# Optimization experiments

Hardware: AMD Instinct MI355X
Metric: run time of the kernel (lower is better)

Reference implementation:

```python
import jax, jax.numpy as jnp
import numpy as np

FT_IN = 40960   # HalfKP-style feature space
FFT_IN = 640    # factorized piece-square features
FT_OUT = 256


def setup_inputs() -> dict:
    key = jax.random.key(0)
    ks = jax.random.split(key, 10)
    B, A = 16384, 30  # batch, active features per board
    inp = {
        "stm_idx": jax.random.randint(ks[0], (B, A), 0, FT_IN, dtype=jnp.int32),
        "nstm_idx": jax.random.randint(ks[1], (B, A), 0, FT_IN, dtype=jnp.int32),
        "f_stm_idx": jax.random.randint(ks[2], (B, A), 0, FFT_IN, dtype=jnp.int32),
        "f_nstm_idx": jax.random.randint(ks[3], (B, A), 0, FFT_IN, dtype=jnp.int32),
        # learned parameters (glorot-ish scale)
        "ft_w": jax.random.normal(ks[4], (FT_IN, FT_OUT), jnp.float32) * 0.01,
        "ft_b": jax.random.normal(ks[5], (FT_OUT,), jnp.float32) * 0.01,
        "fft_w": jax.random.normal(ks[6], (FFT_IN, FT_OUT), jnp.float32) * 0.05,
        "fft_b": jax.random.normal(ks[7], (FT_OUT,), jnp.float32) * 0.01,
        "out_w": jax.random.normal(ks[8], (2 * FT_OUT, 1), jnp.float32) * 0.05,
        "out_b": jax.random.normal(ks[9], (1,), jnp.float32) * 0.01,
    }
    return inp


def _accumulate(w, b, idx):
    # sparse one-hot board @ kernel + bias == gather rows and sum over active features
    return jnp.take(w, idx, axis=0).sum(axis=1) + b  # [B, FT_OUT]


def reference(stm_idx, nstm_idx, f_stm_idx, f_nstm_idx,
              ft_w, ft_b, fft_w, fft_b, out_w, out_b):
    stm = _accumulate(ft_w, ft_b, stm_idx)        # [B, 256]
    nstm = _accumulate(ft_w, ft_b, nstm_idx)      # [B, 256]
    f_stm = _accumulate(fft_w, fft_b, f_stm_idx)  # [B, 256]
    f_nstm = _accumulate(fft_w, fft_b, f_nstm_idx)
    merge = jnp.concatenate((stm, nstm), axis=1) + jnp.concatenate((f_stm, f_nstm), axis=1)
    h = jnp.clip(merge, 0.0, 1.0)                 # ReLU(max_value=1.0)
    return jax.nn.sigmoid(h @ out_w + out_b)      # [B, 1]
```

## Files before the change

### kernel.cpp

```cpp
#include <hip/hip_runtime.h>
#include <math.h>

#define FT_IN  40960
#define FFT_IN 640
#define FT_OUT 256
#define NA     30
#define NSLICE 4
#define BPB    128

typedef float f32x2 __attribute__((ext_vector_type(2)));

__device__ __forceinline__ unsigned enc4(float a, float b, float c, float d) {
    unsigned r = 0;
    r = __builtin_amdgcn_cvt_pk_fp8_f32(a, b, r, false);
    r = __builtin_amdgcn_cvt_pk_fp8_f32(c, d, r, true);
    return r;
}

__device__ __forceinline__ void conv8_block(const float* __restrict__ src,
                                            uint4* __restrict__ dst,
                                            int nrows, int bid, int tid)
{
    int t = bid * 256 + tid;
    int total = nrows * 16;
    if (t >= total) return;
    int r = t >> 4, g = t & 15;
    int s = g >> 2, d = g & 3;
    const float4* sp = (const float4*)(src + (size_t)r * FT_OUT + g * 16);
    float4 v0 = sp[0], v1 = sp[1], v2 = sp[2], v3 = sp[3];
    uint4 u;
    u.x = enc4(v0.x, v0.y, v0.z, v0.w);
    u.y = enc4(v1.x, v1.y, v1.z, v1.w);
    u.z = enc4(v2.x, v2.y, v2.z, v2.w);
    u.w = enc4(v3.x, v3.y, v3.z, v3.w);
    dst[((size_t)s * nrows + r) * 4 + d] = u;
}

__global__ __launch_bounds__(256) void prep(
    const float* __restrict__ ft_w, const float* __restrict__ fft_w,
    const int* __restrict__ stm, const int* __restrict__ nstm,
    const int* __restrict__ fstm, const int* __restrict__ fnstm,
    uint4* __restrict__ ft_o, uint4* __restrict__ fft_o,
    uint2* __restrict__ pidx, int n_boards, int nb_ft, int nb_fft)
{
    int bid = blockIdx.x;
    if (bid < nb_ft) {
        conv8_block(ft_w, ft_o, FT_IN, bid, threadIdx.x);
    } else if (bid < nb_ft + nb_fft) {
        conv8_block(fft_w, fft_o, FFT_IN, bid - nb_ft, threadIdx.x);
    } else {
        int t = (bid - nb_ft - nb_fft) * 256 + (int)threadIdx.x;
        int total = n_boards * NA;
        if (t < total) {
            uint2 v;
            v.x = (unsigned)stm[t]  | ((unsigned)nstm[t]  << 16);
            v.y = (unsigned)fstm[t] | ((unsigned)fnstm[t] << 16);
            pidx[t] = v;
        }
    }
}

__global__ __launch_bounds__(1024, 8) void nnue_gather(
    const uint2* __restrict__ pidx,
    const char* __restrict__ ft, const char* __restrict__ fft,
    const float* __restrict__ ft_b, const float* __restrict__ fft_b,
    const float* __restrict__ out_w, float* __restrict__ partial, int n_boards)
{
    extern __shared__ char smem[];
    uint2* lidx = (uint2*)smem;
    uint2* lf8  = (uint2*)(smem + NA * BPB * 8);
    const int slice = blockIdx.x & (NSLICE - 1);
    const int group = blockIdx.x >> 2;
    const int tid = (int)threadIdx.x;

    {
        const uint2* psrc = pidx + (size_t)group * BPB * NA;
        int lim = (n_boards - group * BPB) * NA;
        if (lim > NA * BPB) lim = NA * BPB;
        for (int i = tid; i < lim; i += 1024)
            lidx[i] = psrc[i];
    }
    {
        const uint2* fsrc = (const uint2*)(fft + (size_t)slice * FFT_IN * 64);
        for (int i = tid; i < FFT_IN * 8; i += 1024) {
            int r = i >> 3, c = i & 7;
            lf8[(r << 3) + ((c + r) & 7)] = fsrc[i];
        }
    }
    __syncthreads();

    const int sub = tid >> 3, ql = tid & 7;
    int board = group * BPB + sub;
    const bool active = board < n_boards;
    const char* ftS = ft + (size_t)slice * FT_IN * 64 + ql * 8;
    const int col = slice * 64 + ql * 8;

    f32x2 a0[4] = {f32x2{0.f,0.f}, f32x2{0.f,0.f}, f32x2{0.f,0.f}, f32x2{0.f,0.f}};
    f32x2 a1[4] = {f32x2{0.f,0.f}, f32x2{0.f,0.f}, f32x2{0.f,0.f}, f32x2{0.f,0.f}};

    const uint2* myidx = lidx + sub * NA;

    #pragma unroll
    for (int a = 0; a < NA; ++a) {
        uint2 iv = myidx[a];
        uint2 u0 = *(const uint2*)(ftS + ((iv.x & 0xFFFFu) << 6));
        uint2 u1 = *(const uint2*)(ftS + ((iv.x >> 16) << 6));
        unsigned rz = iv.y & 0xFFFFu, rw = iv.y >> 16;
        uint2 g0 = lf8[(rz << 3) + (((unsigned)ql + rz) & 7)];
        uint2 g1 = lf8[(rw << 3) + (((unsigned)ql + rw) & 7)];
        a0[0] += __builtin_amdgcn_cvt_pk_f32_fp8(u0.x, false);
        a0[1] += __builtin_amdgcn_cvt_pk_f32_fp8(u0.x, true);
        a0[2] += __builtin_amdgcn_cvt_pk_f32_fp8(u0.y, false);
        a0[3] += __builtin_amdgcn_cvt_pk_f32_fp8(u0.y, true);
        a1[0] += __builtin_amdgcn_cvt_pk_f32_fp8(u1.x, false);
        a1[1] += __builtin_amdgcn_cvt_pk_f32_fp8(u1.x, true);
        a1[2] += __builtin_amdgcn_cvt_pk_f32_fp8(u1.y, false);
        a1[3] += __builtin_amdgcn_cvt_pk_f32_fp8(u1.y, true);
        a0[0] += __builtin_amdgcn_cvt_pk_f32_fp8(g0.x, false);
        a0[1] += __builtin_amdgcn_cvt_pk_f32_fp8(g0.x, true);
        a0[2] += __builtin_amdgcn_cvt_pk_f32_fp8(g0.y, false);
        a0[3] += __builtin_amdgcn_cvt_pk_f32_fp8(g0.y, true);
        a1[0] += __builtin_amdgcn_cvt_pk_f32_fp8(g1.x, false);
        a1[1] += __builtin_amdgcn_cvt_pk_f32_fp8(g1.x, true);
        a1[2] += __builtin_amdgcn_cvt_pk_f32_fp8(g1.y, false);
        a1[3] += __builtin_amdgcn_cvt_pk_f32_fp8(g1.y, true);
    }

    const float4* bfp = (const float4*)(ft_b  + col);
    const float4* bgp = (const float4*)(fft_b + col);
    float4 bf0 = bfp[0], bf1 = bfp[1], bg0 = bgp[0], bg1 = bgp[1];
    float bias[8] = {bf0.x+bg0.x, bf0.y+bg0.y, bf0.z+bg0.z, bf0.w+bg0.w,
                     bf1.x+bg1.x, bf1.y+bg1.y, bf1.z+bg1.z, bf1.w+bg1.w};
    const float4* w0p = (const float4*)(out_w + col);
    const float4* w1p = (const float4*)(out_w + FT_OUT + col);
    float4 w00 = w0p[0], w01 = w0p[1], w10 = w1p[0], w11 = w1p[1];
    float w0[8] = {w00.x, w00.y, w00.z, w00.w, w01.x, w01.y, w01.z, w01.w};
    float w1[8] = {w10.x, w10.y, w10.z, w10.w, w11.x, w11.y, w11.z, w11.w};
    float h0[8], h1[8];
    #pragma unroll
    for (int i = 0; i < 4; ++i) {
        h0[2*i] = a0[i].x; h0[2*i+1] = a0[i].y;
        h1[2*i] = a1[i].x; h1[2*i+1] = a1[i].y;
    }
    float p = 0.f;
    #pragma unroll
    for (int i = 0; i < 8; ++i) {
        p += fminf(fmaxf(h0[i] + bias[i], 0.f), 1.f) * w0[i];
        p += fminf(fmaxf(h1[i] + bias[i], 0.f), 1.f) * w1[i];
    }
    p += __shfl_xor(p, 1, 64);
    p += __shfl_xor(p, 2, 64);
    p += __shfl_xor(p, 4, 64);
    if (active && ql == 0)
        partial[(size_t)slice * n_boards + board] = p;
}

__global__ __launch_bounds__(256) void nnue_final(
    const float* __restrict__ partial, const float* __restrict__ out_b,
    float* __restrict__ out, int n)
{
    int b = blockIdx.x * blockDim.x + threadIdx.x;
    if (b >= n) return;
    float zv = out_b[0];
    #pragma unroll
    for (int s = 0; s < NSLICE; ++s) zv += partial[(size_t)s * n + b];
    out[b] = 1.0f / (1.0f + expf(-zv));
}

__global__ __launch_bounds__(256) void nnue_fwd_direct(
    const int* __restrict__ stm_idx, const int* __restrict__ nstm_idx,
    const int* __restrict__ f_stm_idx, const int* __restrict__ f_nstm_idx,
    const float* __restrict__ ft_w, const float* __restrict__ ft_b,
    const float* __restrict__ fft_w, const float* __restrict__ fft_b,
    const float* __restrict__ out_w, const float* __restrict__ out_b,
    float* __restrict__ out, int n_boards)
{
    const int board = (int)((blockIdx.x * blockDim.x + threadIdx.x) >> 6);
    const int lane  = (int)(threadIdx.x & 63);
    if (board >= n_boards) return;
    const int col = lane << 2;
    const float4 ftb  = *(const float4*)(ft_b  + col);
    const float4 fftb = *(const float4*)(fft_b + col);
    float a0x = ftb.x + fftb.x, a0y = ftb.y + fftb.y,
          a0z = ftb.z + fftb.z, a0w = ftb.w + fftb.w;
    float a1x = a0x, a1y = a0y, a1z = a0z, a1w = a0w;
    const int* si  = stm_idx    + (size_t)board * NA;
    const int* ni  = nstm_idx   + (size_t)board * NA;
    const int* fsi = f_stm_idx  + (size_t)board * NA;
    const int* fni = f_nstm_idx + (size_t)board * NA;
    #pragma unroll 5
    for (int a = 0; a < NA; ++a) {
        const float4 r0 = *(const float4*)(ft_w  + (size_t)si[a]  * FT_OUT + col);
        const float4 r1 = *(const float4*)(ft_w  + (size_t)ni[a]  * FT_OUT + col);
        const float4 r2 = *(const float4*)(fft_w + (size_t)fsi[a] * FT_OUT + col);
        const float4 r3 = *(const float4*)(fft_w + (size_t)fni[a] * FT_OUT + col);
        a0x += r0.x + r2.x; a0y += r0.y + r2.y; a0z += r0.z + r2.z; a0w += r0.w + r2.w;
        a1x += r1.x + r3.x; a1y += r1.y + r3.y; a1z += r1.z + r3.z; a1w += r1.w + r3.w;
    }
    a0x = fminf(fmaxf(a0x, 0.f), 1.f); a0y = fminf(fmaxf(a0y, 0.f), 1.f);
    a0z = fminf(fmaxf(a0z, 0.f), 1.f); a0w = fminf(fmaxf(a0w, 0.f), 1.f);
    a1x = fminf(fmaxf(a1x, 0.f), 1.f); a1y = fminf(fmaxf(a1y, 0.f), 1.f);
    a1z = fminf(fmaxf(a1z, 0.f), 1.f); a1w = fminf(fmaxf(a1w, 0.f), 1.f);
    const float4 w0 = *(const float4*)(out_w + col);
    const float4 w1 = *(const float4*)(out_w + FT_OUT + col);
    float p = a0x * w0.x + a0y * w0.y + a0z * w0.z + a0w * w0.w
            + a1x * w1.x + a1y * w1.y + a1z * w1.z + a1w * w1.w;
    #pragma unroll
    for (int off = 32; off > 0; off >>= 1) p += __shfl_down(p, off, 64);
    if (lane == 0) out[board] = 1.0f / (1.0f + expf(-(p + out_b[0])));
}

extern "C" void kernel_launch(void* const* d_in, const int* in_sizes, int n_in,
                              void* d_out, int out_size, void* d_ws, size_t ws_size,
                              hipStream_t stream) {
    const int*   stm_idx    = (const int*)d_in[0];
    const int*   nstm_idx   = (const int*)d_in[1];
    const int*   f_stm_idx  = (const int*)d_in[2];
    const int*   f_nstm_idx = (const int*)d_in[3];
    const float* ft_w  = (const float*)d_in[4];
    const float* ft_b  = (const float*)d_in[5];
    const float* fft_w = (const float*)d_in[6];
    const float* fft_b = (const float*)d_in[7];
    const float* out_w = (const float*)d_in[8];
    const float* out_b = (const float*)d_in[9];
    float* out = (float*)d_out;

    const int n_boards = in_sizes[0] / NA;

    const size_t ft_bytes   = (size_t)FT_IN  * FT_OUT;
    const size_t fft_bytes  = (size_t)FFT_IN * FT_OUT;
    const size_t pidx_bytes = (size_t)n_boards * NA * sizeof(uint2);
    const size_t part_bytes = (size_t)n_boards * NSLICE * sizeof(float);
    const size_t need = ft_bytes + fft_bytes + pidx_bytes + part_bytes;

    const size_t lds_bytes = (size_t)NA * BPB * 8 + (size_t)FFT_IN * 64;

    bool ok = (ws_size >= need);
    if (ok) {
        ok = (hipFuncSetAttribute((const void*)nnue_gather,
                                  hipFuncAttributeMaxDynamicSharedMemorySize,
                                  (int)lds_bytes) == hipSuccess);
    }
    if (!ok) {
        const int grid = (n_boards + 3) / 4;
        nnue_fwd_direct<<<grid, 256, 0, stream>>>(stm_idx, nstm_idx, f_stm_idx, f_nstm_idx,
                                                  ft_w, ft_b, fft_w, fft_b, out_w, out_b,
                                                  out, n_boards);
        return;
    }

    char* wsp = (char*)d_ws;
    uint4* ws_ft   = (uint4*)wsp;               wsp += ft_bytes;
    uint4* ws_fft  = (uint4*)wsp;               wsp += fft_bytes;
    uint2* ws_pidx = (uint2*)wsp;               wsp += pidx_bytes;
    float* ws_part = (float*)wsp;

    {
        const int nb_ft   = FT_IN  * 16 / 256;
        const int nb_fft  = FFT_IN * 16 / 256;
        const int nb_pack = (n_boards * NA + 255) / 256;
        prep<<<nb_ft + nb_fft + nb_pack, 256, 0, stream>>>(
            ft_w, fft_w, stm_idx, nstm_idx, f_stm_idx, f_nstm_idx,
            ws_ft, ws_fft, ws_pidx, n_boards, nb_ft, nb_fft);
    }
    {
        int groups = (n_boards + BPB - 1) / BPB;
        nnue_gather<<<groups * NSLICE, 1024, lds_bytes, stream>>>(
            (const uint2*)ws_pidx, (const char*)ws_ft, (const char*)ws_fft,
            ft_b, fft_b, out_w, ws_part, n_boards);
    }
    {
        nnue_final<<<(n_boards + 255) / 256, 256, 0, stream>>>(ws_part, out_b, out, n_boards);
    }
}
```

Before: 132.9 us.

## Drop LDS staging of factorized weights and split lanes by side with 16-byte loads

The gather kernel no longer copies the factorized fp8 weight slice into LDS. Instead, each lane loads 16-byte rows of both tables directly from global memory, and lanes are split between the stm and nstm sides, with each lane covering 16 columns of one side. Blocks shrink from 1024 threads and 128 boards to 256 threads and 32 boards, with static LDS used only for indices. This removes the per-block LDS fill of 40KB and the dynamic-LDS setup, and should raise occupancy. The trade-off is that factorized-weight reads now go through L2/L1 instead of LDS.

New measurement: 136.6 us. 2.8% more time.

```diff
diff --git a/kernel.cpp b/kernel.cpp
--- a/kernel.cpp
+++ b/kernel.cpp
@@ -6,7 +6,7 @@
 #define FT_OUT 256
 #define NA     30
 #define NSLICE 4
-#define BPB    128
+#define BPB    32
 
 typedef float f32x2 __attribute__((ext_vector_type(2)));
 
@@ -60,15 +60,13 @@
     }
 }
 
-__global__ __launch_bounds__(1024, 8) void nnue_gather(
+__global__ __launch_bounds__(256, 5) void nnue_gather(
     const uint2* __restrict__ pidx,
     const char* __restrict__ ft, const char* __restrict__ fft,
     const float* __restrict__ ft_b, const float* __restrict__ fft_b,
     const float* __restrict__ out_w, float* __restrict__ partial, int n_boards)
 {
-    extern __shared__ char smem[];
-    uint2* lidx = (uint2*)smem;
-    uint2* lf8  = (uint2*)(smem + NA * BPB * 8);
+    __shared__ uint2 lidx[BPB * NA];
     const int slice = blockIdx.x & (NSLICE - 1);
     const int group = blockIdx.x >> 2;
     const int tid = (int)threadIdx.x;
@@ -77,76 +75,68 @@
         const uint2* psrc = pidx + (size_t)group * BPB * NA;
         int lim = (n_boards - group * BPB) * NA;
         if (lim > NA * BPB) lim = NA * BPB;
-        for (int i = tid; i < lim; i += 1024)
-            lidx[i] = psrc[i];
-    }
-    {
-        const uint2* fsrc = (const uint2*)(fft + (size_t)slice * FFT_IN * 64);
-        for (int i = tid; i < FFT_IN * 8; i += 1024) {
-            int r = i >> 3, c = i & 7;
-            lf8[(r << 3) + ((c + r) & 7)] = fsrc[i];
-        }
+        for (int i = tid; i < NA * BPB; i += 256)
+            lidx[i] = (i < lim) ? psrc[i] : uint2{0u, 0u};
     }
     __syncthreads();
 
-    const int sub = tid >> 3, ql = tid & 7;
-    int board = group * BPB + sub;
+    const int sub  = tid >> 3;
+    const int ql   = tid & 7;
+    const int side = ql >> 2;
+    const int c    = ql & 3;
+    const unsigned shf = (unsigned)side << 4;
+    const int board = group * BPB + sub;
     const bool active = board < n_boards;
-    const char* ftS = ft + (size_t)slice * FT_IN * 64 + ql * 8;
-    const int col = slice * 64 + ql * 8;
-
-    f32x2 a0[4] = {f32x2{0.f,0.f}, f32x2{0.f,0.f}, f32x2{0.f,0.f}, f32x2{0.f,0.f}};
-    f32x2 a1[4] = {f32x2{0.f,0.f}, f32x2{0.f,0.f}, f32x2{0.f,0.f}, f32x2{0.f,0.f}};
+
+    const char* ftS  = ft  + (size_t)slice * FT_IN  * 64 + c * 16;
+    const char* fftS = fft + (size_t)slice * FFT_IN * 64 + c * 16;
+    const int col = slice * 64 + c * 16;
+
+    f32x2 acc[8];
+    #pragma unroll
+    for (int i = 0; i < 8; ++i) acc[i] = f32x2{0.f, 0.f};
 
     const uint2* myidx = lidx + sub * NA;
 
     #pragma unroll
     for (int a = 0; a < NA; ++a) {
         uint2 iv = myidx[a];
-        uint2 u0 = *(const uint2*)(ftS + ((iv.x & 0xFFFFu) << 6));
-        uint2 u1 = *(const uint2*)(ftS + ((iv.x >> 16) << 6));
-        unsigned rz = iv.y & 0xFFFFu, rw = iv.y >> 16;
-        uint2 g0 = lf8[(rz << 3) + (((unsigned)ql + rz) & 7)];
-        uint2 g1 = lf8[(rw << 3) + (((unsigned)ql + rw) & 7)];
-        a0[0] += __builtin_amdgcn_cvt_pk_f32_fp8(u0.x, false);
-        a0[1] += __builtin_amdgcn_cvt_pk_f32_fp8(u0.x, true);
-        a0[2] += __builtin_amdgcn_cvt_pk_f32_fp8(u0.y, false);
-        a0[3] += __builtin_amdgcn_cvt_pk_f32_fp8(u0.y, true);
-        a1[0] += __builtin_amdgcn_cvt_pk_f32_fp8(u1.x, false);
-        a1[1] += __builtin_amdgcn_cvt_pk_f32_fp8(u1.x, true);
-        a1[2] += __builtin_amdgcn_cvt_pk_f32_fp8(u1.y, false);
-        a1[3] += __builtin_amdgcn_cvt_pk_f32_fp8(u1.y, true);
-        a0[0] += __builtin_amdgcn_cvt_pk_f32_fp8(g0.x, false);
-        a0[1] += __builtin_amdgcn_cvt_pk_f32_fp8(g0.x, true);
-        a0[2] += __builtin_amdgcn_cvt_pk_f32_fp8(g0.y, false);
-        a0[3] += __builtin_amdgcn_cvt_pk_f32_fp8(g0.y, true);
-        a1[0] += __builtin_amdgcn_cvt_pk_f32_fp8(g1.x, false);
-        a1[1] += __builtin_amdgcn_cvt_pk_f32_fp8(g1.x, true);
-        a1[2] += __builtin_amdgcn_cvt_pk_f32_fp8(g1.y, false);
-        a1[3] += __builtin_amdgcn_cvt_pk_f32_fp8(g1.y, true);
-    }
-
-    const float4* bfp = (const float4*)(ft_b  + col);
-    const float4* bgp = (const float4*)(fft_b + col);
-    float4 bf0 = bfp[0], bf1 = bfp[1], bg0 = bgp[0], bg1 = bgp[1];
-    float bias[8] = {bf0.x+bg0.x, bf0.y+bg0.y, bf0.z+bg0.z, bf0.w+bg0.w,
-                     bf1.x+bg1.x, bf1.y+bg1.y, bf1.z+bg1.z, bf1.w+bg1.w};
-    const float4* w0p = (const float4*)(out_w + col);
-    const float4* w1p = (const float4*)(out_w + FT_OUT + col);
-    float4 w00 = w0p[0], w01 = w0p[1], w10 = w1p[0], w11 = w1p[1];
-    float w0[8] = {w00.x, w00.y, w00.z, w00.w, w01.x, w01.y, w01.z, w01.w};
-    float w1[8] = {w10.x, w10.y, w10.z, w10.w, w11.x, w11.y, w11.z, w11.w};
-    float h0[8], h1[8];
-    #pragma unroll
-    for (int i = 0; i < 4; ++i) {
-        h0[2*i] = a0[i].x; h0[2*i+1] = a0[i].y;
-        h1[2*i] = a1[i].x; h1[2*i+1] = a1[i].y;
-    }
+        unsigned rx = (iv.x >> shf) & 0xFFFFu;
+        unsigned ry = (iv.y >> shf) & 0xFFFFu;
+        uint4 u = *(const uint4*)(ftS  + ((size_t)rx << 6));
+        uint4 g = *(const uint4*)(fftS + ((size_t)ry << 6));
+        acc[0] += __builtin_amdgcn_cvt_pk_f32_fp8(u.x, false);
+        acc[1] += __builtin_amdgcn_cvt_pk_f32_fp8(u.x, true);
+        acc[2] += __builtin_amdgcn_cvt_pk_f32_fp8(u.y, false);
+        acc[3] += __builtin_amdgcn_cvt_pk_f32_fp8(u.y, true);
+        acc[4] += __builtin_amdgcn_cvt_pk_f32_fp8(u.z, false);
+        acc[5] += __builtin_amdgcn_cvt_pk_f32_fp8(u.z, true);
+        acc[6] += __builtin_amdgcn_cvt_pk_f32_fp8(u.w, false);
+        acc[7] += __builtin_amdgcn_cvt_pk_f32_fp8(u.w, true);
+        acc[0] += __builtin_amdgcn_cvt_pk_f32_fp8(g.x, false);
+        acc[1] += __builtin_amdgcn_cvt_pk_f32_fp8(g.x, true);
+        acc[2] += __builtin_amdgcn_cvt_pk_f32_fp8(g.y, false);
+        acc[3] += __builtin_amdgcn_cvt_pk_f32_fp8(g.y, true);
+        acc[4] += __builtin_amdgcn_cvt_pk_f32_fp8(g.z, false);
+        acc[5] += __builtin_amdgcn_cvt_pk_f32_fp8(g.z, true);
+        acc[6] += __builtin_amdgcn_cvt_pk_f32_fp8(g.w, false);
+        acc[7] += __builtin_amdgcn_cvt_pk_f32_fp8(g.w, true);
+    }
+
+    float h[16];
+    #pragma unroll
+    for (int i = 0; i < 8; ++i) { h[2*i] = acc[i].x; h[2*i+1] = acc[i].y; }
+    const float4* bf = (const float4*)(ft_b  + col);
+    const float4* bg = (const float4*)(fft_b + col);
+    const float4* wp = (const float4*)(out_w + side * FT_OUT + col);
     float p = 0.f;
     #pragma unroll
-    for (int i = 0; i < 8; ++i) {
-        p += fminf(fmaxf(h0[i] + bias[i], 0.f), 1.f) * w0[i];
-        p += fminf(fmaxf(h1[i] + bias[i], 0.f), 1.f) * w1[i];
+    for (int q = 0; q < 4; ++q) {
+        float4 b = bf[q], gq = bg[q], w = wp[q];
+        p += fminf(fmaxf(h[4*q+0] + b.x + gq.x, 0.f), 1.f) * w.x;
+        p += fminf(fmaxf(h[4*q+1] + b.y + gq.y, 0.f), 1.f) * w.y;
+        p += fminf(fmaxf(h[4*q+2] + b.z + gq.z, 0.f), 1.f) * w.z;
+        p += fminf(fmaxf(h[4*q+3] + b.w + gq.w, 0.f), 1.f) * w.w;
     }
     p += __shfl_xor(p, 1, 64);
     p += __shfl_xor(p, 2, 64);
@@ -233,15 +223,7 @@
     const size_t part_bytes = (size_t)n_boards * NSLICE * sizeof(float);
     const size_t need = ft_bytes + fft_bytes + pidx_bytes + part_bytes;
 
-    const size_t lds_bytes = (size_t)NA * BPB * 8 + (size_t)FFT_IN * 64;
-
-    bool ok = (ws_size >= need);
-    if (ok) {
-        ok = (hipFuncSetAttribute((const void*)nnue_gather,
-                                  hipFuncAttributeMaxDynamicSharedMemorySize,
-                                  (int)lds_bytes) == hipSuccess);
-    }
-    if (!ok) {
+    if (ws_size < need) {
         const int grid = (n_boards + 3) / 4;
         nnue_fwd_direct<<<grid, 256, 0, stream>>>(stm_idx, nstm_idx, f_stm_idx, f_nstm_idx,
                                                   ft_w, ft_b, fft_w, fft_b, out_w, out_b,
@@ -265,7 +247,7 @@
     }
     {
         int groups = (n_boards + BPB - 1) / BPB;
-        nnue_gather<<<groups * NSLICE, 1024, lds_bytes, stream>>>(
+        nnue_gather<<<groups * NSLICE, 256, 0, stream>>>(
             (const uint2*)ws_pidx, (const char*)ws_ft, (const char*)ws_fft,
             ft_b, fft_b, out_w, ws_part, n_boards);
     }
```
